# Optimization experiments

Measured on AMD Instinct MI355X. Metric: run time of the kernel, lower is better.

## Reference

```python
import jax, jax.numpy as jnp
import numpy as np

REP_THR = 0.6
BORDER = 10


def setup_inputs() -> dict:
    key = jax.random.key(0)
    repeatability = jax.random.uniform(key, (8, 1, 2048, 2048), dtype=jnp.float32)
    return {"repeatability": repeatability}


def reference(repeatability):
    # 3x3 max pool, stride 1, pad 1 (torch pads with -inf for max pool)
    local_max = jax.lax.reduce_window(
        repeatability,
        -jnp.inf,
        jax.lax.max,
        window_dimensions=(1, 1, 3, 3),
        window_strides=(1, 1, 1, 1),
        padding=[(0, 0), (0, 0), (1, 1), (1, 1)],
    )
    maxima = (repeatability == local_max) & (repeatability >= REP_THR)
    # border mask: zero out a 10-pixel frame
    B, C, H, W = repeatability.shape
    border = jnp.zeros((H, W), dtype=bool).at[BORDER:-BORDER, BORDER:-BORDER].set(True)
    maxima = maxima & border  # broadcast over (B, C)
    # Original returns maxima.nonzero().t()[2:4] (data-dependent shape);
    # for jit-compatibility we return the dense boolean mask as float32 —
    # the (y, x) indices are exactly the nonzero positions of this mask.
    return maxima.astype(jnp.float32)
```

## Files before the change

### kernel.cpp

```cpp
#include <hip/hip_runtime.h>
#include <math.h>

#define IMG_H 2048
#define IMG_W 2048
#define NB    8
#define BORDER 10
#define REP_THR 0.6f

typedef float f32x4 __attribute__((ext_vector_type(4)));

__global__ __launch_bounds__(256) void nms_kernel(const float* __restrict__ in,
                                                  float* __restrict__ out) {
    const int orig = blockIdx.x;
    const int swz  = (orig & 7) * 4096 + (orig >> 3);
    const int tid  = (swz << 8) | threadIdx.x;

    const int gx = tid & 511;
    const int y  = (tid >> 9) & 2047;
    const int b  = tid >> 20;

    const int x4 = gx << 2;

    const size_t img_off = (size_t)b * IMG_H * IMG_W;
    float* optr = out + img_off + (size_t)y * IMG_W + x4;

    if (y < BORDER || y >= IMG_H - BORDER || gx == 0 || gx == 511) {
        const f32x4 z = {0.f, 0.f, 0.f, 0.f};
        *(f32x4*)optr = z;
        return;
    }

    const float* base = in + img_off + (size_t)y * IMG_W + x4;
    const float* r0 = base - IMG_W;
    const float* r1 = base;
    const float* r2 = base + IMG_W;

    const f32x4 v0 = *(const f32x4*)r0;
    const f32x4 v1 = *(const f32x4*)r1;
    const f32x4 v2 = *(const f32x4*)r2;
    const float l0 = r0[-1], q0 = r0[4];
    const float l1 = r1[-1], q1 = r1[4];
    const float l2 = r2[-1], q2 = r2[4];

    f32x4 h0, h1, h2;
    h0[0] = fmaxf(l0,    fmaxf(v0[0], v0[1]));
    h0[1] = fmaxf(v0[0], fmaxf(v0[1], v0[2]));
    h0[2] = fmaxf(v0[1], fmaxf(v0[2], v0[3]));
    h0[3] = fmaxf(v0[2], fmaxf(v0[3], q0));
    h1[0] = fmaxf(l1,    fmaxf(v1[0], v1[1]));
    h1[1] = fmaxf(v1[0], fmaxf(v1[1], v1[2]));
    h1[2] = fmaxf(v1[1], fmaxf(v1[2], v1[3]));
    h1[3] = fmaxf(v1[2], fmaxf(v1[3], q1));
    h2[0] = fmaxf(l2,    fmaxf(v2[0], v2[1]));
    h2[1] = fmaxf(v2[0], fmaxf(v2[1], v2[2]));
    h2[2] = fmaxf(v2[1], fmaxf(v2[2], v2[3]));
    h2[3] = fmaxf(v2[2], fmaxf(v2[3], q2));

    f32x4 m;
    m[0] = fmaxf(h0[0], fmaxf(h1[0], h2[0]));
    m[1] = fmaxf(h0[1], fmaxf(h1[1], h2[1]));
    m[2] = fmaxf(h0[2], fmaxf(h1[2], h2[2]));
    m[3] = fmaxf(h0[3], fmaxf(h1[3], h2[3]));

    const bool bx0 = (x4 + 0 >= BORDER) && (x4 + 0 < IMG_W - BORDER);
    const bool bx1 = (x4 + 1 >= BORDER) && (x4 + 1 < IMG_W - BORDER);
    const bool bx2 = (x4 + 2 >= BORDER) && (x4 + 2 < IMG_W - BORDER);
    const bool bx3 = (x4 + 3 >= BORDER) && (x4 + 3 < IMG_W - BORDER);

    f32x4 r;
    r[0] = (v1[0] == m[0] && v1[0] >= REP_THR && bx0) ? 1.f : 0.f;
    r[1] = (v1[1] == m[1] && v1[1] >= REP_THR && bx1) ? 1.f : 0.f;
    r[2] = (v1[2] == m[2] && v1[2] >= REP_THR && bx2) ? 1.f : 0.f;
    r[3] = (v1[3] == m[3] && v1[3] >= REP_THR && bx3) ? 1.f : 0.f;

    *(f32x4*)optr = r;
}

extern "C" void kernel_launch(void* const* d_in, const int* in_sizes, int n_in,
                              void* d_out, int out_size, void* d_ws, size_t ws_size,
                              hipStream_t stream) {
    const float* in = (const float*)d_in[0];
    float* out = (float*)d_out;
    const int total_threads = NB * IMG_H * (IMG_W / 4);
    const int block = 256;
    const int grid = total_threads / block;
    nms_kernel<<<grid, block, 0, stream>>>(in, out);
}
```

Before: 229.9 us.

## Process 64-row strips per thread with rolling horizontal-max window and prefetch

Each thread now walks a vertical strip of 64 rows instead of producing one row. It keeps a rotating set of four horizontal-max vectors, so every input row is loaded once rather than three times, and it prefetches two rows ahead, with sched_barriers to keep loads issued early. Row indices are clamped and border rows are masked inside the loop, which removes the early-exit branch. The cost is a much smaller grid of 512 blocks doing long sequential loops, which leaves less thread-level parallelism to hide memory latency.

```diff
diff --git a/kernel.cpp b/kernel.cpp
--- a/kernel.cpp
+++ b/kernel.cpp
@@ -6,74 +6,105 @@
 #define NB    8
 #define BORDER 10
 #define REP_THR 0.6f
+#define SH 64
 
 typedef float f32x4 __attribute__((ext_vector_type(4)));
 
-__global__ __launch_bounds__(256) void nms_kernel(const float* __restrict__ in,
-                                                  float* __restrict__ out) {
+__global__ __launch_bounds__(256, 2) void nms_kernel(const float* __restrict__ in,
+                                                     float* __restrict__ out) {
     const int orig = blockIdx.x;
-    const int swz  = (orig & 7) * 4096 + (orig >> 3);
-    const int tid  = (swz << 8) | threadIdx.x;
+    const int swz  = (orig & 7) * 64 + (orig >> 3);
+    const int tid  = (swz << 8) | (int)threadIdx.x;
 
-    const int gx = tid & 511;
-    const int y  = (tid >> 9) & 2047;
-    const int b  = tid >> 20;
+    const int gx    = tid & 511;
+    const int strip = (tid >> 9) & 31;
+    const int b     = tid >> 14;
 
     const int x4 = gx << 2;
+    const int y0 = strip << 6;
 
     const size_t img_off = (size_t)b * IMG_H * IMG_W;
-    float* optr = out + img_off + (size_t)y * IMG_W + x4;
-
-    if (y < BORDER || y >= IMG_H - BORDER || gx == 0 || gx == 511) {
-        const f32x4 z = {0.f, 0.f, 0.f, 0.f};
-        *(f32x4*)optr = z;
-        return;
-    }
-
-    const float* base = in + img_off + (size_t)y * IMG_W + x4;
-    const float* r0 = base - IMG_W;
-    const float* r1 = base;
-    const float* r2 = base + IMG_W;
-
-    const f32x4 v0 = *(const f32x4*)r0;
-    const f32x4 v1 = *(const f32x4*)r1;
-    const f32x4 v2 = *(const f32x4*)r2;
-    const float l0 = r0[-1], q0 = r0[4];
-    const float l1 = r1[-1], q1 = r1[4];
-    const float l2 = r2[-1], q2 = r2[4];
-
-    f32x4 h0, h1, h2;
-    h0[0] = fmaxf(l0,    fmaxf(v0[0], v0[1]));
-    h0[1] = fmaxf(v0[0], fmaxf(v0[1], v0[2]));
-    h0[2] = fmaxf(v0[1], fmaxf(v0[2], v0[3]));
-    h0[3] = fmaxf(v0[2], fmaxf(v0[3], q0));
-    h1[0] = fmaxf(l1,    fmaxf(v1[0], v1[1]));
-    h1[1] = fmaxf(v1[0], fmaxf(v1[1], v1[2]));
-    h1[2] = fmaxf(v1[1], fmaxf(v1[2], v1[3]));
-    h1[3] = fmaxf(v1[2], fmaxf(v1[3], q1));
-    h2[0] = fmaxf(l2,    fmaxf(v2[0], v2[1]));
-    h2[1] = fmaxf(v2[0], fmaxf(v2[1], v2[2]));
-    h2[2] = fmaxf(v2[1], fmaxf(v2[2], v2[3]));
-    h2[3] = fmaxf(v2[2], fmaxf(v2[3], q2));
-
-    f32x4 m;
-    m[0] = fmaxf(h0[0], fmaxf(h1[0], h2[0]));
-    m[1] = fmaxf(h0[1], fmaxf(h1[1], h2[1]));
-    m[2] = fmaxf(h0[2], fmaxf(h1[2], h2[2]));
-    m[3] = fmaxf(h0[3], fmaxf(h1[3], h2[3]));
+    const float* ibase = in  + img_off + x4;
+    float*       obase = out + img_off + (size_t)y0 * IMG_W + x4;
 
     const bool bx0 = (x4 + 0 >= BORDER) && (x4 + 0 < IMG_W - BORDER);
     const bool bx1 = (x4 + 1 >= BORDER) && (x4 + 1 < IMG_W - BORDER);
     const bool bx2 = (x4 + 2 >= BORDER) && (x4 + 2 < IMG_W - BORDER);
     const bool bx3 = (x4 + 3 >= BORDER) && (x4 + 3 < IMG_W - BORDER);
 
-    f32x4 r;
-    r[0] = (v1[0] == m[0] && v1[0] >= REP_THR && bx0) ? 1.f : 0.f;
-    r[1] = (v1[1] == m[1] && v1[1] >= REP_THR && bx1) ? 1.f : 0.f;
-    r[2] = (v1[2] == m[2] && v1[2] >= REP_THR && bx2) ? 1.f : 0.f;
-    r[3] = (v1[3] == m[3] && v1[3] >= REP_THR && bx3) ? 1.f : 0.f;
+#define CLAMPR(r) ((r) < (BORDER - 1) ? (BORDER - 1) \
+                 : ((r) > (IMG_H - BORDER) ? (IMG_H - BORDER) : (r)))
 
-    *(f32x4*)optr = r;
+#define ISSUE(row, V, L, Q) do {                                  \
+        const float* _p = ibase + (size_t)CLAMPR(row) * IMG_W;    \
+        (V) = *(const f32x4*)_p;                                  \
+        (L) = _p[-1];                                             \
+        (Q) = _p[4];                                              \
+    } while (0)
+
+#define HMAX(H, V, L, Q) do {                                     \
+        (H)[0] = fmaxf((L),    fmaxf((V)[0], (V)[1]));            \
+        (H)[1] = fmaxf((V)[0], fmaxf((V)[1], (V)[2]));            \
+        (H)[2] = fmaxf((V)[1], fmaxf((V)[2], (V)[3]));            \
+        (H)[3] = fmaxf((V)[2], fmaxf((V)[3], (V)[3] > (Q) ? (Q) : (Q))); \
+    } while (0)
+
+#undef HMAX
+#define HMAX(H, V, L, Q) do {                                     \
+        (H)[0] = fmaxf((L),    fmaxf((V)[0], (V)[1]));            \
+        (H)[1] = fmaxf((V)[0], fmaxf((V)[1], (V)[2]));            \
+        (H)[2] = fmaxf((V)[1], fmaxf((V)[2], (V)[3]));            \
+        (H)[3] = fmaxf((V)[2], fmaxf((V)[3], (Q)));               \
+    } while (0)
+
+    f32x4 vA, vB, vC;
+    float lA, qA, lB, qB, lC, qC;
+    ISSUE(y0 - 1, vA, lA, qA);
+    ISSUE(y0 + 0, vB, lB, qB);
+    ISSUE(y0 + 1, vC, lC, qC);
+
+    f32x4 pV0; float pL0, pQ0;
+    f32x4 pV1; float pL1, pQ1;
+    ISSUE(y0 + 2, pV0, pL0, pQ0);
+    ISSUE(y0 + 3, pV1, pL1, pQ1);
+
+    f32x4 hS0, hS1, hS2, hS3;
+    HMAX(hS0, vA, lA, qA);
+    HMAX(hS1, vB, lB, qB);
+    HMAX(hS2, vC, lC, qC);
+    f32x4 vs0 = vB;
+    f32x4 vs1 = vC;
+
+#define ITER(j, Hm1, H0, Hp1, Hp2, PV, PL, PQ, VS) do {                   \
+        const int _y = y0 + (j);                                          \
+        f32x4 _m;                                                         \
+        _m[0] = fmaxf((Hm1)[0], fmaxf((H0)[0], (Hp1)[0]));                \
+        _m[1] = fmaxf((Hm1)[1], fmaxf((H0)[1], (Hp1)[1]));                \
+        _m[2] = fmaxf((Hm1)[2], fmaxf((H0)[2], (Hp1)[2]));                \
+        _m[3] = fmaxf((Hm1)[3], fmaxf((H0)[3], (Hp1)[3]));                \
+        const bool _rowok = (_y >= BORDER) && (_y < IMG_H - BORDER);      \
+        f32x4 _r;                                                         \
+        _r[0] = ((VS)[0] == _m[0] && (VS)[0] >= REP_THR && bx0 && _rowok) ? 1.f : 0.f; \
+        _r[1] = ((VS)[1] == _m[1] && (VS)[1] >= REP_THR && bx1 && _rowok) ? 1.f : 0.f; \
+        _r[2] = ((VS)[2] == _m[2] && (VS)[2] >= REP_THR && bx2 && _rowok) ? 1.f : 0.f; \
+        _r[3] = ((VS)[3] == _m[3] && (VS)[3] >= REP_THR && bx3 && _rowok) ? 1.f : 0.f; \
+        *(f32x4*)(obase + (size_t)(j) * IMG_W) = _r;                      \
+        HMAX((Hp2), (PV), (PL), (PQ));     \
+        (VS) = (PV);                       \
+        ISSUE((j) + y0 + 4, (PV), (PL), (PQ));    \
+        __builtin_amdgcn_sched_barrier(0);                                \
+    } while (0)
+
+    for (int j = 0; j < SH; j += 4) {
+        ITER(j + 0, hS0, hS1, hS2, hS3, pV0, pL0, pQ0, vs0);
+        ITER(j + 1, hS1, hS2, hS3, hS0, pV1, pL1, pQ1, vs1);
+        ITER(j + 2, hS2, hS3, hS0, hS1, pV0, pL0, pQ0, vs0);
+        ITER(j + 3, hS3, hS0, hS1, hS2, pV1, pL1, pQ1, vs1);
+    }
+#undef ITER
+#undef ISSUE
+#undef HMAX
+#undef CLAMPR
 }
 
 extern "C" void kernel_launch(void* const* d_in, const int* in_sizes, int n_in,
@@ -81,7 +112,7 @@
                               hipStream_t stream) {
     const float* in = (const float*)d_in[0];
     float* out = (float*)d_out;
-    const int total_threads = NB * IMG_H * (IMG_W / 4);
+    const int total_threads = NB * (IMG_H / SH) * (IMG_W / 4);
     const int block = 256;
     const int grid = total_threads / block;
     nms_kernel<<<grid, block, 0, stream>>>(in, out);
```

New measurement: 240.9 us. +4.8%, slower.
